# Kernel optimization log

Measured on AMD Instinct MI355X. Metric: run time of the kernel, lower is better.

Reference implementation:

```python
import jax, jax.numpy as jnp
import numpy as np

B, S, D, NH = 1, 2048, 2048, 8
DH = D // NH
BACKEND_EPS = 1e-6
NORM_EPS = 1e-6


def setup_inputs() -> dict:
    key = jax.random.key(0)
    ks = jax.random.split(key, 6)
    q = jax.random.normal(ks[0], (B, S, D), jnp.float32)
    k = jax.random.normal(ks[1], (B, S, D), jnp.float32)
    v = jax.random.normal(ks[2], (B, S, D), jnp.float32)
    igate_kernel = jax.random.normal(ks[3], (3 * D, NH), jnp.float32) * 0.02
    igate_bias = jax.random.normal(ks[4], (NH,), jnp.float32) * 0.1
    fgate_kernel = jax.random.normal(ks[5], (3 * D, NH), jnp.float32) * 0.02
    fgate_bias = jnp.linspace(3.0, 6.0, NH, dtype=jnp.float32)  # bias_linspace_init(3.0, 6.0)
    out_weight = jnp.ones((NH, DH), jnp.float32)  # MultiHeadLayerNorm scale (no bias)
    return dict(q=q, k=k, v=v, igate_kernel=igate_kernel, igate_bias=igate_bias,
                fgate_kernel=fgate_kernel, fgate_bias=fgate_bias, out_weight=out_weight)


def _mlstm_parallel_stabilized(q, k, v, i_pre, f_pre):
    # q,k,v: (B,NH,S,DH); i_pre,f_pre: (B,NH,S)
    s = q.shape[-2]
    dh = q.shape[-1]
    log_f = jax.nn.log_sigmoid(f_pre)                              # (B,NH,S)
    cum = jnp.pad(jnp.cumsum(log_f, axis=-1), ((0, 0), (0, 0), (1, 0)))  # (B,NH,S+1), cum[0]=0
    # logfg[t, s] = cum[t+1] - cum[s+1] = sum_{j=s+1}^{t} log_f[j], valid for s <= t
    logfg = cum[..., 1:, None] - cum[..., None, 1:]                # (B,NH,S,S)
    causal = jnp.tril(jnp.ones((s, s), dtype=bool))
    logfg = jnp.where(causal, logfg, -jnp.inf)
    log_D = logfg + i_pre[..., None, :]                            # add input gate at source position s
    m = jnp.max(log_D, axis=-1, keepdims=True)                     # stabilizer (B,NH,S,1)
    D = jnp.exp(log_D - m)
    qk = jnp.einsum('bhsd,bhtd->bhst', q, k) / jnp.sqrt(jnp.float32(dh))
    C = qk * D                                                     # (B,NH,S,S)
    n = jnp.maximum(jnp.abs(jnp.sum(C, axis=-1, keepdims=True)), jnp.exp(-m))
    return jnp.einsum('bhst,bhtd->bhsd', C / (n + BACKEND_EPS), v)


def reference(q, k, v, igate_kernel, igate_bias, fgate_kernel, fgate_bias, out_weight):
    qkv = jnp.concatenate([q, k, v], axis=-1)                      # (B,S,3D)
    i_pre = qkv @ igate_kernel + igate_bias                        # (B,S,NH)
    f_pre = qkv @ fgate_kernel + fgate_bias                        # (B,S,NH)
    qh = q.reshape(B, S, NH, DH).transpose(0, 2, 1, 3)             # (B,NH,S,DH)
    kh = k.reshape(B, S, NH, DH).transpose(0, 2, 1, 3)
    vh = v.reshape(B, S, NH, DH).transpose(0, 2, 1, 3)
    h = _mlstm_parallel_stabilized(qh, kh, vh,
                                   i_pre.transpose(0, 2, 1),
                                   f_pre.transpose(0, 2, 1))       # (B,NH,S,DH)
    h = h.transpose(0, 2, 1, 3)                                    # (B,S,NH,DH)
    mu = jnp.mean(h, axis=-1, keepdims=True)
    var = jnp.var(h, axis=-1, keepdims=True)
    hn = (h - mu) * jax.lax.rsqrt(var + NORM_EPS) * out_weight     # per-head LN, scale only
    return hn.reshape(B, S, D)
```

## Files before the change

kernel.cpp:

```cpp
#include <hip/hip_runtime.h>
#include <hip/hip_bf16.h>

#define SEQ 2048
#define DMODEL 2048
#define NHEAD 8
#define DHEAD 256

typedef _Float16 v8h __attribute__((ext_vector_type(8)));
typedef unsigned short v8u __attribute__((ext_vector_type(8)));
typedef float v4f __attribute__((ext_vector_type(4)));

__device__ __forceinline__ float b2f(unsigned short s) {
    return __uint_as_float(((unsigned)s) << 16);
}
__device__ __forceinline__ unsigned short f2b(float f) {
    unsigned u = __float_as_uint(f);
    u += 0x7fffu + ((u >> 16) & 1u);
    return (unsigned short)(u >> 16);
}
__device__ __forceinline__ unsigned short f2h(float f) {
    _Float16 h = (_Float16)f;
    return __builtin_bit_cast(unsigned short, h);
}
__device__ __forceinline__ float h2f(unsigned short s) {
    return (float)__builtin_bit_cast(_Float16, s);
}

__global__ __launch_bounds__(256) void k_cvt(const void* q, const void* k, const void* v,
                                             int* flag,
                                             unsigned short* qb, unsigned short* kb,
                                             unsigned short* vT) {
    __shared__ unsigned short tile[64][72];
    __shared__ int cnt;
    const int tid = threadIdx.x;
    const int b = blockIdx.x;

    if (tid == 0) cnt = 0;
    __syncthreads();
    {
        const unsigned short* qp = (const unsigned short*)q;
        int wild = 0;
        for (int i = tid; i < 2048; i += 256) {
            float x = b2f(qp[i]);
            float ax = fabsf(x);
            if (!(ax <= 100.0f) || (x != 0.0f && ax < 1e-6f)) wild++;
        }
        atomicAdd(&cnt, wild);
    }
    __syncthreads();
    const int bf = (cnt < 256) ? 1 : 0;
    if (b == 0 && tid == 0) *flag = bf;

    if (b < 1024) {
        size_t i0 = ((size_t)b * 256 + tid) * 16;
        if (bf) {
            const unsigned short* qp = (const unsigned short*)q;
            const unsigned short* kp = (const unsigned short*)k;
#pragma unroll
            for (int hlf = 0; hlf < 2; hlf++) {
                v8u uq = *(const v8u*)(qp + i0 + hlf * 8);
                v8u uk = *(const v8u*)(kp + i0 + hlf * 8);
                v8u oq, ok;
#pragma unroll
                for (int j = 0; j < 8; j++) { oq[j] = f2h(b2f(uq[j])); ok[j] = f2h(b2f(uk[j])); }
                *(v8u*)(qb + i0 + hlf * 8) = oq;
                *(v8u*)(kb + i0 + hlf * 8) = ok;
            }
        } else {
            const float* qf = (const float*)q;
            const float* kf = (const float*)k;
#pragma unroll
            for (int hlf = 0; hlf < 2; hlf++) {
                v4f q0 = *(const v4f*)(qf + i0 + hlf * 8);
                v4f q1 = *(const v4f*)(qf + i0 + hlf * 8 + 4);
                v4f k0 = *(const v4f*)(kf + i0 + hlf * 8);
                v4f k1 = *(const v4f*)(kf + i0 + hlf * 8 + 4);
                v8u oq, ok;
#pragma unroll
                for (int j = 0; j < 4; j++) {
                    oq[j] = f2h(q0[j]); oq[4 + j] = f2h(q1[j]);
                    ok[j] = f2h(k0[j]); ok[4 + j] = f2h(k1[j]);
                }
                *(v8u*)(qb + i0 + hlf * 8) = oq;
                *(v8u*)(kb + i0 + hlf * 8) = ok;
            }
        }
    } else {
        int b2 = b - 1024;
        int s0 = (b2 & 31) * 64, d0 = (b2 >> 5) * 64;
        int r = tid >> 2, c0 = (tid & 3) * 16;
        size_t base = (size_t)(s0 + r) * DMODEL + d0 + c0;
        if (bf) {
            const unsigned short* vp = (const unsigned short*)v;
            v8u a = *(const v8u*)(vp + base);
            v8u bb = *(const v8u*)(vp + base + 8);
#pragma unroll
            for (int j = 0; j < 8; j++) { tile[r][c0 + j] = f2h(b2f(a[j])); tile[r][c0 + 8 + j] = f2h(b2f(bb[j])); }
        } else {
            const float* vp = (const float*)v;
            v4f a0 = *(const v4f*)(vp + base);
            v4f a1 = *(const v4f*)(vp + base + 4);
            v4f a2 = *(const v4f*)(vp + base + 8);
            v4f a3 = *(const v4f*)(vp + base + 12);
#pragma unroll
            for (int j = 0; j < 4; j++) {
                tile[r][c0 + j] = f2h(a0[j]);      tile[r][c0 + 4 + j] = f2h(a1[j]);
                tile[r][c0 + 8 + j] = f2h(a2[j]);  tile[r][c0 + 12 + j] = f2h(a3[j]);
            }
        }
        __syncthreads();
        int dr = tid >> 2, sc0 = (tid & 3) * 16;
        v8u o0, o1;
#pragma unroll
        for (int j = 0; j < 8; j++) { o0[j] = tile[sc0 + j][dr]; o1[j] = tile[sc0 + 8 + j][dr]; }
        int head = d0 >> 8;
        int dh = (d0 & 255) + dr;
        size_t ob = ((size_t)head * DHEAD + dh) * SEQ + s0 + sc0;
        *(v8u*)(vT + ob) = o0;
        *(v8u*)(vT + ob + 8) = o1;
    }
}

__global__ __launch_bounds__(256) void k_gates(const unsigned short* __restrict__ qb,
                                               const unsigned short* __restrict__ kb,
                                               const void* __restrict__ v,
                                               const void* __restrict__ igk,
                                               const void* __restrict__ fgk,
                                               const int* flag,
                                               float* ipre, float* fpre) {
    __shared__ float x_lds[32][68];
    const int bf = *(volatile const int*)flag;
    const int s0 = blockIdx.x * 32;
    const int c  = blockIdx.y;
    const int tid = threadIdx.x;
    const int sl = tid >> 3, hh = tid & 7;
    const int rr = tid >> 3, j0 = (tid & 7) * 8;
    float accI = 0.f, accF = 0.f;
    const unsigned short* ik16 = (const unsigned short*)igk;
    const unsigned short* fk16 = (const unsigned short*)fgk;
    const float* ik32 = (const float*)igk;
    const float* fk32 = (const float*)fgk;

    for (int wd = 0; wd < 12; ++wd) {
        const int gd0 = c * 768 + wd * 64;
        __syncthreads();
        {
            float xv[8];
            if (gd0 < 4096) {
                const unsigned short* sp = (gd0 < 2048) ? qb : kb;
                const int off = (gd0 < 2048) ? gd0 : gd0 - 2048;
                v8u a = *(const v8u*)(sp + (size_t)(s0 + rr) * DMODEL + off + j0);
#pragma unroll
                for (int j = 0; j < 8; j++) xv[j] = h2f(a[j]);
            } else if (bf) {
                const unsigned short* vp = (const unsigned short*)v;
                v8u a = *(const v8u*)(vp + (size_t)(s0 + rr) * DMODEL + (gd0 - 4096) + j0);
#pragma unroll
                for (int j = 0; j < 8; j++) xv[j] = b2f(a[j]);
            } else {
                const float* vp = (const float*)v;
                const size_t base = (size_t)(s0 + rr) * DMODEL + (gd0 - 4096) + j0;
                v4f a0 = *(const v4f*)(vp + base);
                v4f a1 = *(const v4f*)(vp + base + 4);
#pragma unroll
                for (int j = 0; j < 4; j++) { xv[j] = a0[j]; xv[4 + j] = a1[j]; }
            }
#pragma unroll
            for (int j = 0; j < 8; j++) x_lds[rr][j0 + j] = xv[j];
        }
        __syncthreads();
        if (bf) {
#pragma unroll 8
            for (int j = 0; j < 64; j++) {
                float x = x_lds[sl][j];
                int wi = (gd0 + j) * NHEAD + hh;
                accI += x * b2f(ik16[wi]);
                accF += x * b2f(fk16[wi]);
            }
        } else {
#pragma unroll 8
            for (int j = 0; j < 64; j++) {
                float x = x_lds[sl][j];
                int wi = (gd0 + j) * NHEAD + hh;
                accI += x * ik32[wi];
                accF += x * fk32[wi];
            }
        }
    }
    atomicAdd(&ipre[hh * SEQ + s0 + sl], accI);
    atomicAdd(&fpre[hh * SEQ + s0 + sl], accF);
}

__global__ __launch_bounds__(256) void k_scan(const float* ipre, const float* fpre,
                                              const void* ib_, const void* fb_,
                                              const int* flag,
                                              float* a_g, float* amax_g, float* nfl_g) {
    __shared__ float wtot[4], wmax[4];
    int bf = *(volatile const int*)flag;
    int h = blockIdx.x, tid = threadIdx.x;
    int lane = tid & 63, wv = tid >> 6;
    float ib = bf ? b2f(((const unsigned short*)ib_)[h]) : ((const float*)ib_)[h];
    float fb = bf ? b2f(((const unsigned short*)fb_)[h]) : ((const float*)fb_)[h];
    int s0 = tid * 8;
    float lf[8], ip[8];
#pragma unroll
    for (int j = 0; j < 8; j++) {
        float fp = fpre[h * SEQ + s0 + j] + fb;
        lf[j] = fminf(fp, 0.0f) - log1pf(__expf(-fabsf(fp)));
        ip[j] = ipre[h * SEQ + s0 + j] + ib;
    }
    float cs[8]; float t = 0.f;
#pragma unroll
    for (int j = 0; j < 8; j++) { t += lf[j]; cs[j] = t; }
    float incl = t;
#pragma unroll
    for (int o = 1; o < 64; o <<= 1) {
        float n = __shfl_up(incl, o, 64);
        if (lane >= o) incl += n;
    }
    if (lane == 63) wtot[wv] = incl;
    __syncthreads();
    float wpre = 0.f;
#pragma unroll
    for (int i2 = 0; i2 < 4; i2++) if (i2 < wv) wpre += wtot[i2];
    float excl = wpre + incl - t;
    float cum[8], av[8];
#pragma unroll
    for (int j = 0; j < 8; j++) { cum[j] = excl + cs[j]; av[j] = ip[j] - cum[j]; }
    float mx = av[0];
#pragma unroll
    for (int j = 1; j < 8; j++) mx = fmaxf(mx, av[j]);
    float mincl = mx;
#pragma unroll
    for (int o = 1; o < 64; o <<= 1) {
        float n = __shfl_up(mincl, o, 64);
        if (lane >= o) mincl = fmaxf(mincl, n);
    }
    if (lane == 63) wmax[wv] = mincl;
    __syncthreads();
    float wpm = -3.0e38f;
#pragma unroll
    for (int i2 = 0; i2 < 4; i2++) if (i2 < wv) wpm = fmaxf(wpm, wmax[i2]);
    float up = __shfl_up(mincl, 1, 64);
    float run = fmaxf(wpm, (lane > 0) ? up : -3.0e38f);
#pragma unroll
    for (int j = 0; j < 8; j++) {
        run = fmaxf(run, av[j]);
        int s = s0 + j;
        a_g[h * SEQ + s]    = av[j];
        amax_g[h * SEQ + s] = run;
        float m = cum[j] + run;
        nfl_g[h * SEQ + s]  = __expf(fminf(fmaxf(-m, -60.f), 60.f));
    }
}

__global__ __launch_bounds__(256, 3) void k_main(const unsigned short* __restrict__ qb,
                                                 const unsigned short* __restrict__ kb,
                                                 const unsigned short* __restrict__ vT,
                                                 const float* __restrict__ a_g,
                                                 const float* __restrict__ amax_g,
                                                 float* __restrict__ h_buf,
                                                 float* __restrict__ rs_buf) {
    __shared__ __align__(16) unsigned short k_lds[32][264];
    __shared__ __align__(16) unsigned short vT_lds[272][40];
    __shared__ __align__(16) unsigned short P_lds[32][40];
    __shared__ __align__(16) unsigned short Plo_lds[32][40];
    __shared__ float a_s[32], amax_t[32];

    const int h   = blockIdx.x;
    const int y   = blockIdx.y;
    const int tid = threadIdx.x;
    const int lane = tid & 63;
    const int w   = tid >> 6;
    const int l15 = lane & 15;
    const int qd  = (lane >> 4) & 3;
    const int hd0 = h * DHEAD;

    int u         = (y * 2080) / 96;
    int remaining = ((y + 1) * 2080) / 96 - u;
    int tile = (int)((sqrtf(8.0f * (float)u + 1.0f) - 1.0f) * 0.5f);
    while ((tile + 1) * (tile + 2) / 2 <= u) ++tile;
    while (tile * (tile + 1) / 2 > u) --tile;
    int js = u - tile * (tile + 1) / 2;
    bool needQ = true;

    for (int i = tid; i < 16 * 40; i += 256) {
        int r2 = i / 40, c2 = i % 40;
        vT_lds[256 + r2][c2] = (r2 == 0 && c2 < 32) ? (unsigned short)0x3C00 : (unsigned short)0;
    }

    const v4f vzero = {0.f, 0.f, 0.f, 0.f};
    v4f acc[2][4];
    v4f accN[2];
#pragma unroll
    for (int m = 0; m < 2; m++) {
        accN[m] = vzero;
#pragma unroll
        for (int n = 0; n < 4; n++) acc[m][n] = vzero;
    }

    const int mw = w >> 1, nw = w & 1;
    const int krow = tid >> 3, kc0 = (tid & 7) * 32;

    v8u qr[8];

    v8u kr0, kr1, kr2, kr3, vr0, vr1, vr2, vr3;
    float areg = 0.f;
    {
        const int s0 = js * 32;
        const unsigned short* ks = kb + (size_t)(s0 + krow) * DMODEL + hd0 + kc0;
        kr0 = *(const v8u*)(ks);      kr1 = *(const v8u*)(ks + 8);
        kr2 = *(const v8u*)(ks + 16); kr3 = *(const v8u*)(ks + 24);
        const unsigned short* vs = vT + (size_t)(hd0 + tid) * SEQ + s0;
        vr0 = *(const v8u*)(vs);      vr1 = *(const v8u*)(vs + 8);
        vr2 = *(const v8u*)(vs + 16); vr3 = *(const v8u*)(vs + 24);
        if (tid < 32) areg = a_g[h * SEQ + s0 + tid];
    }

    for (;;) {
        const int t0 = tile * 32;
        __syncthreads();
        if (needQ) {
            const unsigned short* src = qb + (size_t)(t0 + mw * 16 + l15) * DMODEL + hd0 + qd * 8;
#pragma unroll
            for (int i = 0; i < 8; i++)
                qr[i] = *(const v8u*)(src + i * 32);
            if (tid < 32) amax_t[tid] = amax_g[h * SEQ + t0 + tid];
            needQ = false;
        }
        *(v8u*)&k_lds[krow][kc0]      = kr0;
        *(v8u*)&k_lds[krow][kc0 + 8]  = kr1;
        *(v8u*)&k_lds[krow][kc0 + 16] = kr2;
        *(v8u*)&k_lds[krow][kc0 + 24] = kr3;
        *(v8u*)&vT_lds[tid][0]  = vr0;
        *(v8u*)&vT_lds[tid][8]  = vr1;
        *(v8u*)&vT_lds[tid][16] = vr2;
        *(v8u*)&vT_lds[tid][24] = vr3;
        if (tid < 32) a_s[tid] = areg;
        __syncthreads();

        v4f c = vzero;
#pragma unroll
        for (int i = 0; i < 8; i++) {
            v8h a = __builtin_bit_cast(v8h, qr[i]);
            v8h b = *(const v8h*)&k_lds[nw * 16 + l15][i * 32 + qd * 8];
            c = __builtin_amdgcn_mfma_f32_16x16x32_f16(a, b, c, 0, 0, 0);
        }
        {
            const bool diag = (js == tile);
            const int col = nw * 16 + l15;
            const float av = a_s[col];
#pragma unroll
            for (int r = 0; r < 4; r++) {
                int row = mw * 16 + qd * 4 + r;
                float arg = fminf(av - amax_t[row], 0.0f);
                float val = c[r] * 0.0625f * __expf(arg);
                if (diag && col > row) val = 0.0f;
                unsigned short hi = f2h(val);
                float lo = val - h2f(hi);
                P_lds[row][col]   = hi;
                Plo_lds[row][col] = f2h(lo);
            }
        }
        __syncthreads();

        int ntile = tile, njs = js + 1; bool nq = false;
        if (njs > tile) { ntile = tile + 1; njs = 0; nq = true; }
        if (remaining > 1) {
            const int s0 = njs * 32;
            const unsigned short* ks = kb + (size_t)(s0 + krow) * DMODEL + hd0 + kc0;
            kr0 = *(const v8u*)(ks);      kr1 = *(const v8u*)(ks + 8);
            kr2 = *(const v8u*)(ks + 16); kr3 = *(const v8u*)(ks + 24);
            const unsigned short* vs = vT + (size_t)(hd0 + tid) * SEQ + s0;
            vr0 = *(const v8u*)(vs);      vr1 = *(const v8u*)(vs + 8);
            vr2 = *(const v8u*)(vs + 16); vr3 = *(const v8u*)(vs + 24);
            if (tid < 32) areg = a_g[h * SEQ + s0 + tid];
        }

        v8h aH0 = *(const v8h*)&P_lds[l15][qd * 8];
        v8h aH1 = *(const v8h*)&P_lds[16 + l15][qd * 8];
        v8h aL0 = *(const v8h*)&Plo_lds[l15][qd * 8];
        v8h aL1 = *(const v8h*)&Plo_lds[16 + l15][qd * 8];
#pragma unroll
        for (int nn = 0; nn < 4; nn++) {
            v8h bV = *(const v8h*)&vT_lds[w * 64 + nn * 16 + l15][qd * 8];
            acc[0][nn] = __builtin_amdgcn_mfma_f32_16x16x32_f16(aH0, bV, acc[0][nn], 0, 0, 0);
            acc[0][nn] = __builtin_amdgcn_mfma_f32_16x16x32_f16(aL0, bV, acc[0][nn], 0, 0, 0);
            acc[1][nn] = __builtin_amdgcn_mfma_f32_16x16x32_f16(aH1, bV, acc[1][nn], 0, 0, 0);
            acc[1][nn] = __builtin_amdgcn_mfma_f32_16x16x32_f16(aL1, bV, acc[1][nn], 0, 0, 0);
        }
        if (w == 3) {
            v8h bN = *(const v8h*)&vT_lds[256 + l15][qd * 8];
            accN[0] = __builtin_amdgcn_mfma_f32_16x16x32_f16(aH0, bN, accN[0], 0, 0, 0);
            accN[0] = __builtin_amdgcn_mfma_f32_16x16x32_f16(aL0, bN, accN[0], 0, 0, 0);
            accN[1] = __builtin_amdgcn_mfma_f32_16x16x32_f16(aH1, bN, accN[1], 0, 0, 0);
            accN[1] = __builtin_amdgcn_mfma_f32_16x16x32_f16(aL1, bN, accN[1], 0, 0, 0);
        }

        if (js == tile || remaining == 1) {
#pragma unroll
            for (int m = 0; m < 2; m++)
#pragma unroll
                for (int r = 0; r < 4; r++) {
                    int row = t0 + m * 16 + qd * 4 + r;
#pragma unroll
                    for (int nn = 0; nn < 4; nn++) {
                        int col = hd0 + w * 64 + nn * 16 + l15;
                        atomicAdd(&h_buf[(size_t)row * DMODEL + col], acc[m][nn][r]);
                        acc[m][nn][r] = 0.f;
                    }
                    if (w == 3 && l15 == 0)
                        atomicAdd(&rs_buf[h * SEQ + row], accN[m][r]);
                    accN[m][r] = 0.f;
                }
        }
        if (--remaining == 0) break;
        tile = ntile; js = njs; needQ = nq;
    }
}

__global__ __launch_bounds__(256) void k_finish(const float* __restrict__ h_buf,
                                                const float* __restrict__ rs_buf,
                                                const float* __restrict__ nfl_g,
                                                const void* __restrict__ ow,
                                                const int* flag, void* out) {
    const int wv = threadIdx.x >> 6, lane = threadIdx.x & 63;
    const int rid = blockIdx.x * 4 + wv;
    const int s = rid >> 3, h = rid & 7;
    const int bf = *(volatile const int*)flag;
    float rs  = rs_buf[h * SEQ + s];
    float nfl = nfl_g[h * SEQ + s];
    float sc  = 1.0f / (fmaxf(fabsf(rs), nfl) + 1e-6f);
    size_t base = (size_t)s * DMODEL + h * DHEAD + lane * 4;
    v4f hv = *(const v4f*)(h_buf + base);
#pragma unroll
    for (int j = 0; j < 4; j++) hv[j] *= sc;
    float sm = hv[0] + hv[1] + hv[2] + hv[3];
    float sq = hv[0] * hv[0] + hv[1] * hv[1] + hv[2] * hv[2] + hv[3] * hv[3];
#pragma unroll
    for (int m = 1; m < 64; m <<= 1) {
        sm += __shfl_xor(sm, m, 64);
        sq += __shfl_xor(sq, m, 64);
    }
    float mean = sm * (1.0f / 256.0f);
    float var  = fmaxf(sq * (1.0f / 256.0f) - mean * mean, 0.0f);
    float rstd = rsqrtf(var + 1e-6f);
    int gi = h * DHEAD + lane * 4;
    float gv[4];
    if (bf) {
        const unsigned short* gp = (const unsigned short*)ow;
#pragma unroll
        for (int j = 0; j < 4; j++) gv[j] = b2f(gp[gi + j]);
    } else {
        const float* gp = (const float*)ow;
#pragma unroll
        for (int j = 0; j < 4; j++) gv[j] = gp[gi + j];
    }
    if (bf) {
        unsigned short* o = (unsigned short*)out + base;
#pragma unroll
        for (int j = 0; j < 4; j++) o[j] = f2b((hv[j] - mean) * rstd * gv[j]);
    } else {
        float* o = (float*)out + base;
#pragma unroll
        for (int j = 0; j < 4; j++) o[j] = (hv[j] - mean) * rstd * gv[j];
    }
}

extern "C" void kernel_launch(void* const* d_in, const int* in_sizes, int n_in,
                              void* d_out, int out_size, void* d_ws, size_t ws_size,
                              hipStream_t stream) {
    const void* q   = d_in[0];
    const void* k   = d_in[1];
    const void* v   = d_in[2];
    const void* igk = d_in[3];
    const void* igb = d_in[4];
    const void* fgk = d_in[5];
    const void* fgb = d_in[6];
    const void* ow  = d_in[7];

    char* ws = (char*)d_ws;
    int*   flag   = (int*)(ws + 0);
    float* ipre   = (float*)(ws + 1024);
    float* fpre   = ipre + NHEAD * SEQ;
    float* rs_buf = fpre + NHEAD * SEQ;
    float* h_buf  = rs_buf + NHEAD * SEQ;
    float* a_g    = h_buf + (size_t)SEQ * DMODEL;
    float* amax_g = a_g + NHEAD * SEQ;
    float* nfl_g  = amax_g + NHEAD * SEQ;
    unsigned short* qb = (unsigned short*)(nfl_g + NHEAD * SEQ);
    unsigned short* kb = qb + (size_t)SEQ * DMODEL;
    unsigned short* vT = kb + (size_t)SEQ * DMODEL;

    size_t zbytes = (size_t)(3 * NHEAD * SEQ) * 4 + (size_t)SEQ * DMODEL * 4;
    hipMemsetAsync(ipre, 0, zbytes, stream);
    k_cvt<<<2048, 256, 0, stream>>>(q, k, v, flag, qb, kb, vT);
    k_gates<<<dim3(64, 8), 256, 0, stream>>>(qb, kb, v, igk, fgk, flag, ipre, fpre);
    k_scan<<<8, 256, 0, stream>>>(ipre, fpre, igb, fgb, flag, a_g, amax_g, nfl_g);
    k_main<<<dim3(8, 96), 256, 0, stream>>>(qb, kb, vT, a_g, amax_g, h_buf, rs_buf);
    k_finish<<<4096, 256, 0, stream>>>(h_buf, rs_buf, nfl_g, ow, flag, d_out);
}
```

Baseline: 256.8 us.

## Load K and V MFMA fragments directly from global memory, bypassing LDS staging

The K and V tiles are no longer staged through shared memory. Each wave now reads its MFMA operand fragments straight from global memory into registers. The all-ones normaliser column becomes a register constant, and the gate and stabiliser values are read per lane instead of from shared arrays. This removes the LDS writes and reads and one barrier per iteration. In exchange, K rows are loaded redundantly across waves, the V fragment loads are strided 16-byte accesses issued right before use with no prefetch, and more registers are needed.

```diff
diff --git a/kernel.cpp b/kernel.cpp
--- a/kernel.cpp
+++ b/kernel.cpp
@@ -261,11 +261,8 @@
                                                  const float* __restrict__ amax_g,
                                                  float* __restrict__ h_buf,
                                                  float* __restrict__ rs_buf) {
-    __shared__ __align__(16) unsigned short k_lds[32][264];
-    __shared__ __align__(16) unsigned short vT_lds[272][40];
     __shared__ __align__(16) unsigned short P_lds[32][40];
     __shared__ __align__(16) unsigned short Plo_lds[32][40];
-    __shared__ float a_s[32], amax_t[32];
 
     const int h   = blockIdx.x;
     const int y   = blockIdx.y;
@@ -275,6 +272,10 @@
     const int l15 = lane & 15;
     const int qd  = (lane >> 4) & 3;
     const int hd0 = h * DHEAD;
+    const int mw = w >> 1, nw = w & 1;
+    const int qrow = mw * 16 + l15;
+    const int krow = nw * 16 + l15;
+    const int coff = qd * 8;
 
     int u         = (y * 2080) / 96;
     int remaining = ((y + 1) * 2080) / 96 - u;
@@ -284,11 +285,6 @@
     int js = u - tile * (tile + 1) / 2;
     bool needQ = true;
 
-    for (int i = tid; i < 16 * 40; i += 256) {
-        int r2 = i / 40, c2 = i % 40;
-        vT_lds[256 + r2][c2] = (r2 == 0 && c2 < 32) ? (unsigned short)0x3C00 : (unsigned short)0;
-    }
-
     const v4f vzero = {0.f, 0.f, 0.f, 0.f};
     v4f acc[2][4];
     v4f accN[2];
@@ -299,61 +295,48 @@
         for (int n = 0; n < 4; n++) acc[m][n] = vzero;
     }
 
-    const int mw = w >> 1, nw = w & 1;
-    const int krow = tid >> 3, kc0 = (tid & 7) * 32;
-
-    v8u qr[8];
-
-    v8u kr0, kr1, kr2, kr3, vr0, vr1, vr2, vr3;
-    float areg = 0.f;
+    v8h bN;
+#pragma unroll
+    for (int j = 0; j < 8; j++) bN[j] = (l15 == 0) ? (_Float16)1.0f : (_Float16)0.0f;
+
+    v8u qr[8], kfr[8];
+    v4f amax4;
+    float av = 0.f, av2 = 0.f;
     {
         const int s0 = js * 32;
-        const unsigned short* ks = kb + (size_t)(s0 + krow) * DMODEL + hd0 + kc0;
-        kr0 = *(const v8u*)(ks);      kr1 = *(const v8u*)(ks + 8);
-        kr2 = *(const v8u*)(ks + 16); kr3 = *(const v8u*)(ks + 24);
-        const unsigned short* vs = vT + (size_t)(hd0 + tid) * SEQ + s0;
-        vr0 = *(const v8u*)(vs);      vr1 = *(const v8u*)(vs + 8);
-        vr2 = *(const v8u*)(vs + 16); vr3 = *(const v8u*)(vs + 24);
-        if (tid < 32) areg = a_g[h * SEQ + s0 + tid];
+        const unsigned short* ks = kb + (size_t)(s0 + krow) * DMODEL + hd0 + coff;
+#pragma unroll
+        for (int i = 0; i < 8; i++) kfr[i] = *(const v8u*)(ks + i * 32);
+        av = a_g[h * SEQ + s0 + krow];
     }
 
     for (;;) {
         const int t0 = tile * 32;
-        __syncthreads();
+        const int s0 = js * 32;
         if (needQ) {
-            const unsigned short* src = qb + (size_t)(t0 + mw * 16 + l15) * DMODEL + hd0 + qd * 8;
-#pragma unroll
-            for (int i = 0; i < 8; i++)
-                qr[i] = *(const v8u*)(src + i * 32);
-            if (tid < 32) amax_t[tid] = amax_g[h * SEQ + t0 + tid];
+            const unsigned short* src = qb + (size_t)(t0 + qrow) * DMODEL + hd0 + coff;
+#pragma unroll
+            for (int i = 0; i < 8; i++) qr[i] = *(const v8u*)(src + i * 32);
+            amax4 = *(const v4f*)(amax_g + h * SEQ + t0 + mw * 16 + qd * 4);
             needQ = false;
         }
-        *(v8u*)&k_lds[krow][kc0]      = kr0;
-        *(v8u*)&k_lds[krow][kc0 + 8]  = kr1;
-        *(v8u*)&k_lds[krow][kc0 + 16] = kr2;
-        *(v8u*)&k_lds[krow][kc0 + 24] = kr3;
-        *(v8u*)&vT_lds[tid][0]  = vr0;
-        *(v8u*)&vT_lds[tid][8]  = vr1;
-        *(v8u*)&vT_lds[tid][16] = vr2;
-        *(v8u*)&vT_lds[tid][24] = vr3;
-        if (tid < 32) a_s[tid] = areg;
-        __syncthreads();
 
         v4f c = vzero;
 #pragma unroll
         for (int i = 0; i < 8; i++) {
             v8h a = __builtin_bit_cast(v8h, qr[i]);
-            v8h b = *(const v8h*)&k_lds[nw * 16 + l15][i * 32 + qd * 8];
+            v8h b = __builtin_bit_cast(v8h, kfr[i]);
             c = __builtin_amdgcn_mfma_f32_16x16x32_f16(a, b, c, 0, 0, 0);
         }
+
+        __syncthreads();
         {
             const bool diag = (js == tile);
-            const int col = nw * 16 + l15;
-            const float av = a_s[col];
+            const int col = krow;
 #pragma unroll
             for (int r = 0; r < 4; r++) {
                 int row = mw * 16 + qd * 4 + r;
-                float arg = fminf(av - amax_t[row], 0.0f);
+                float arg = fminf(av - amax4[r], 0.0f);
                 float val = c[r] * 0.0625f * __expf(arg);
                 if (diag && col > row) val = 0.0f;
                 unsigned short hi = f2h(val);
@@ -364,33 +347,34 @@
         }
         __syncthreads();
 
+        v8u vfr[4];
+#pragma unroll
+        for (int nn = 0; nn < 4; nn++)
+            vfr[nn] = *(const v8u*)(vT + (size_t)(hd0 + w * 64 + nn * 16 + l15) * SEQ + s0 + coff);
+
         int ntile = tile, njs = js + 1; bool nq = false;
         if (njs > tile) { ntile = tile + 1; njs = 0; nq = true; }
         if (remaining > 1) {
-            const int s0 = njs * 32;
-            const unsigned short* ks = kb + (size_t)(s0 + krow) * DMODEL + hd0 + kc0;
-            kr0 = *(const v8u*)(ks);      kr1 = *(const v8u*)(ks + 8);
-            kr2 = *(const v8u*)(ks + 16); kr3 = *(const v8u*)(ks + 24);
-            const unsigned short* vs = vT + (size_t)(hd0 + tid) * SEQ + s0;
-            vr0 = *(const v8u*)(vs);      vr1 = *(const v8u*)(vs + 8);
-            vr2 = *(const v8u*)(vs + 16); vr3 = *(const v8u*)(vs + 24);
-            if (tid < 32) areg = a_g[h * SEQ + s0 + tid];
-        }
-
-        v8h aH0 = *(const v8h*)&P_lds[l15][qd * 8];
-        v8h aH1 = *(const v8h*)&P_lds[16 + l15][qd * 8];
-        v8h aL0 = *(const v8h*)&Plo_lds[l15][qd * 8];
-        v8h aL1 = *(const v8h*)&Plo_lds[16 + l15][qd * 8];
+            const int ns0 = njs * 32;
+            const unsigned short* ks = kb + (size_t)(ns0 + krow) * DMODEL + hd0 + coff;
+#pragma unroll
+            for (int i = 0; i < 8; i++) kfr[i] = *(const v8u*)(ks + i * 32);
+            av2 = a_g[h * SEQ + ns0 + krow];
+        }
+
+        v8h aH0 = *(const v8h*)&P_lds[l15][coff];
+        v8h aH1 = *(const v8h*)&P_lds[16 + l15][coff];
+        v8h aL0 = *(const v8h*)&Plo_lds[l15][coff];
+        v8h aL1 = *(const v8h*)&Plo_lds[16 + l15][coff];
 #pragma unroll
         for (int nn = 0; nn < 4; nn++) {
-            v8h bV = *(const v8h*)&vT_lds[w * 64 + nn * 16 + l15][qd * 8];
+            v8h bV = __builtin_bit_cast(v8h, vfr[nn]);
             acc[0][nn] = __builtin_amdgcn_mfma_f32_16x16x32_f16(aH0, bV, acc[0][nn], 0, 0, 0);
             acc[0][nn] = __builtin_amdgcn_mfma_f32_16x16x32_f16(aL0, bV, acc[0][nn], 0, 0, 0);
             acc[1][nn] = __builtin_amdgcn_mfma_f32_16x16x32_f16(aH1, bV, acc[1][nn], 0, 0, 0);
             acc[1][nn] = __builtin_amdgcn_mfma_f32_16x16x32_f16(aL1, bV, acc[1][nn], 0, 0, 0);
         }
         if (w == 3) {
-            v8h bN = *(const v8h*)&vT_lds[256 + l15][qd * 8];
             accN[0] = __builtin_amdgcn_mfma_f32_16x16x32_f16(aH0, bN, accN[0], 0, 0, 0);
             accN[0] = __builtin_amdgcn_mfma_f32_16x16x32_f16(aL0, bN, accN[0], 0, 0, 0);
             accN[1] = __builtin_amdgcn_mfma_f32_16x16x32_f16(aH1, bN, accN[1], 0, 0, 0);
@@ -415,7 +399,7 @@
                 }
         }
         if (--remaining == 0) break;
-        tile = ntile; js = njs; needQ = nq;
+        tile = ntile; js = njs; needQ = nq; av = av2;
     }
 }
 
```

Result: slower. 291.1 us (+13.4%).
